# Kernel tuning notes

Hardware: AMD Instinct MI355X
Metric: run time of the kernel (lower is better)

The kernel has to match this reference:

```python
import jax, jax.numpy as jnp
import numpy as np

N_NODES = 50000
N_FEAT = 128
HIDDEN = 3
N_EDGES = 600000
N_POWERS = 3


def setup_inputs() -> dict:
    key = jax.random.key(0)
    ks = jax.random.split(key, 6)
    x = jax.random.normal(ks[0], (N_NODES, N_FEAT), dtype=jnp.float32)
    edge_index = jax.random.randint(ks[1], (N_POWERS, 2, N_EDGES), 0, N_NODES, dtype=jnp.int64)
    # MLP params for the 3 adjacency powers, stacked on the leading axis.
    # torch Linear(in,out) stored transposed here: y = x @ W + b.
    Wa = jax.random.normal(ks[2], (N_POWERS, N_FEAT, HIDDEN), dtype=jnp.float32) * (1.0 / np.sqrt(N_FEAT))
    ba = jax.random.normal(ks[3], (N_POWERS, HIDDEN), dtype=jnp.float32) * 0.01
    Wb = jax.random.normal(ks[4], (N_POWERS, HIDDEN, 1), dtype=jnp.float32) * (1.0 / np.sqrt(HIDDEN))
    bb = jax.random.normal(ks[5], (N_POWERS, 1), dtype=jnp.float32) * 0.01
    return {"x": x, "edge_index": edge_index, "Wa": Wa, "ba": ba, "Wb": Wb, "bb": bb}


def reference(x, edge_index, Wa, ba, Wb, bb):
    # Gather source/target node features per edge, per adjacency power.
    x_j = x[edge_index[:, 0]]          # [P, E, F]
    x_i = x[edge_index[:, 1]]          # [P, E, F]
    abs_dif = jnp.abs(x_j - x_i)       # [P, E, F]
    # Tiny per-edge MLP: Linear -> ReLU -> Linear -> Sigmoid (separate params per power).
    h = jax.nn.relu(jnp.einsum('pef,pfh->peh', abs_dif, Wa) + ba[:, None, :])  # [P, E, H]
    w = jax.nn.sigmoid(jnp.einsum('peh,pho->peo', h, Wb) + bb[:, None, :])     # [P, E, 1]
    return w[..., 0]                   # [P, E] edge weights for each power
```

## Files before the change

### kernel.cpp

```cpp
#include <hip/hip_runtime.h>
#include <math.h>

#define N_NODES 50000
#define N_FEAT  128
#define N_EDGES 600000
#define N_POWERS 3

#define ITERS 25
#define EDGES_PER_BLK (32 * ITERS)

typedef _Float16 half2v __attribute__((ext_vector_type(2)));
union HU { unsigned u; half2v h; };

__global__ __launch_bounds__(256) void conv_x(const float* __restrict__ x,
                                              unsigned* __restrict__ xh) {
    const int t = blockIdx.x * 256 + threadIdx.x;
    const float4* x4 = (const float4*)x;
    float4 a = x4[(size_t)t * 2];
    float4 b = x4[(size_t)t * 2 + 1];
    HU p0, p1, p2, p3;
    p0.h = half2v{(_Float16)a.x, (_Float16)a.y};
    p1.h = half2v{(_Float16)a.z, (_Float16)a.w};
    p2.h = half2v{(_Float16)b.x, (_Float16)b.y};
    p3.h = half2v{(_Float16)b.z, (_Float16)b.w};
    ((uint4*)xh)[t] = uint4{p0.u, p1.u, p2.u, p3.u};
}

__global__ __launch_bounds__(192) void conv_wa(const float* __restrict__ Wa,
                                               unsigned* __restrict__ wah) {
    const int t = blockIdx.x * 192 + threadIdx.x;
    const int c  = t % 3;
    const int pk = t / 3;
    const int k  = pk % 64;
    const int p  = pk / 64;
    float w0 = Wa[p * 384 + (2 * k) * 3 + c];
    float w1 = Wa[p * 384 + (2 * k + 1) * 3 + c];
    HU u; u.h = half2v{(_Float16)w0, (_Float16)w1};
    wah[t] = u.u;
}

template<int PAT>
__device__ __forceinline__ float swz(float v) {
    return __int_as_float(__builtin_amdgcn_ds_swizzle(__float_as_int(v), PAT));
}

__global__ __launch_bounds__(256) void adj_kernel_f16(
    const unsigned* __restrict__ xh,
    const unsigned* __restrict__ wah,
    const int*   __restrict__ edge_index,
    const float* __restrict__ ba,
    const float* __restrict__ Wb,
    const float* __restrict__ bb,
    float* __restrict__ out)
{
    const int p    = blockIdx.y;
    const int tid  = threadIdx.x;
    const int lane = tid & 63;
    const int wave = tid >> 6;
    const int sub  = lane & 7;
    const int grp  = lane >> 3;

    HU wa[8][3];
    {
        const unsigned* wp = wah + ((size_t)p * 64 + sub * 8) * 3;
        #pragma unroll
        for (int k = 0; k < 8; ++k) {
            wa[k][0].u = wp[k * 3 + 0];
            wa[k][1].u = wp[k * 3 + 1];
            wa[k][2].u = wp[k * 3 + 2];
        }
    }

    const float ba0 = ba[p * 3 + 0], ba1 = ba[p * 3 + 1], ba2 = ba[p * 3 + 2];
    const float wb0 = Wb[p * 3 + 0], wb1 = Wb[p * 3 + 1], wb2 = Wb[p * 3 + 2];
    const float bbp = bb[p];

    const int* ej = edge_index + (size_t)p * 2 * N_EDGES;
    const int* ei = ej + N_EDGES;
    float* outp = out + (size_t)p * N_EDGES;

    const int e_blk = blockIdx.x * EDGES_PER_BLK;
    const int eoff  = wave * 8 + grp;
    const int roff  = sub * 8;

    for (int it = 0; it < ITERS; ++it) {
        const int e = e_blk + it * 32 + eoff;
        const int j = ej[e];
        const int i = ei[e];

        const unsigned* rj = xh + (size_t)j * 64 + roff;
        const unsigned* ri = xh + (size_t)i * 64 + roff;
        uint4 qa0 = *(const uint4*)(rj);
        uint4 qa1 = *(const uint4*)(rj + 4);
        uint4 qb0 = *(const uint4*)(ri);
        uint4 qb1 = *(const uint4*)(ri + 4);

        unsigned ua[8] = {qa0.x, qa0.y, qa0.z, qa0.w, qa1.x, qa1.y, qa1.z, qa1.w};
        unsigned ub[8] = {qb0.x, qb0.y, qb0.z, qb0.w, qb1.x, qb1.y, qb1.z, qb1.w};

        float h0 = 0.f, h1 = 0.f, h2 = 0.f;
        #pragma unroll
        for (int k = 0; k < 8; ++k) {
            HU a, b, d;
            a.u = ua[k]; b.u = ub[k];
            d.h = a.h - b.h;
            d.u &= 0x7fff7fffu;
            h0 = __builtin_amdgcn_fdot2(d.h, wa[k][0].h, h0, false);
            h1 = __builtin_amdgcn_fdot2(d.h, wa[k][1].h, h1, false);
            h2 = __builtin_amdgcn_fdot2(d.h, wa[k][2].h, h2, false);
        }

        h0 += swz<0x041F>(h0); h1 += swz<0x041F>(h1); h2 += swz<0x041F>(h2);
        h0 += swz<0x081F>(h0); h1 += swz<0x081F>(h1); h2 += swz<0x081F>(h2);
        h0 += swz<0x101F>(h0); h1 += swz<0x101F>(h1); h2 += swz<0x101F>(h2);

        if (sub == 0) {
            float r0 = fmaxf(h0 + ba0, 0.f);
            float r1 = fmaxf(h1 + ba1, 0.f);
            float r2 = fmaxf(h2 + ba2, 0.f);
            float s  = fmaf(r0, wb0, fmaf(r1, wb1, fmaf(r2, wb2, bbp)));
            outp[e] = 1.f / (1.f + expf(-s));
        }
    }
}

__global__ __launch_bounds__(256) void adj_kernel_f32(
    const float* __restrict__ x,
    const int*   __restrict__ edge_index,
    const float* __restrict__ Wa,
    const float* __restrict__ ba,
    const float* __restrict__ Wb,
    const float* __restrict__ bb,
    float* __restrict__ out)
{
    const int p    = blockIdx.y;
    const int tid  = threadIdx.x;
    const int lane = tid & 63;
    const int wave = tid >> 6;
    const int sub  = lane & 15;
    const int grp  = lane >> 4;
    const int f0 = sub * 8;

    const float* Wap = Wa + (size_t)p * N_FEAT * 3;
    float wa0[8], wa1[8], wa2[8];
    #pragma unroll
    for (int k = 0; k < 8; ++k) {
        wa0[k] = Wap[(f0 + k) * 3 + 0];
        wa1[k] = Wap[(f0 + k) * 3 + 1];
        wa2[k] = Wap[(f0 + k) * 3 + 2];
    }
    const float ba0 = ba[p * 3 + 0], ba1 = ba[p * 3 + 1], ba2 = ba[p * 3 + 2];
    const float wb0 = Wb[p * 3 + 0], wb1 = Wb[p * 3 + 1], wb2 = Wb[p * 3 + 2];
    const float bbp = bb[p];

    const int e = blockIdx.x * 16 + wave * 4 + grp;
    const int* ej = edge_index + (size_t)p * 2 * N_EDGES;
    const int* ei = ej + N_EDGES;
    const int j = ej[e];
    const int i = ei[e];

    const float4* xj = (const float4*)(x + (size_t)j * N_FEAT + f0);
    const float4* xi = (const float4*)(x + (size_t)i * N_FEAT + f0);
    float4 a0 = xj[0], a1 = xj[1];
    float4 b0 = xi[0], b1 = xi[1];

    float d[8];
    d[0] = fabsf(a0.x - b0.x); d[1] = fabsf(a0.y - b0.y);
    d[2] = fabsf(a0.z - b0.z); d[3] = fabsf(a0.w - b0.w);
    d[4] = fabsf(a1.x - b1.x); d[5] = fabsf(a1.y - b1.y);
    d[6] = fabsf(a1.z - b1.z); d[7] = fabsf(a1.w - b1.w);

    float h0 = 0.f, h1 = 0.f, h2 = 0.f;
    #pragma unroll
    for (int k = 0; k < 8; ++k) {
        h0 = fmaf(d[k], wa0[k], h0);
        h1 = fmaf(d[k], wa1[k], h1);
        h2 = fmaf(d[k], wa2[k], h2);
    }
    #pragma unroll
    for (int m = 1; m < 16; m <<= 1) {
        h0 += __shfl_xor(h0, m, 64);
        h1 += __shfl_xor(h1, m, 64);
        h2 += __shfl_xor(h2, m, 64);
    }
    if (sub == 0) {
        float r0 = fmaxf(h0 + ba0, 0.f);
        float r1 = fmaxf(h1 + ba1, 0.f);
        float r2 = fmaxf(h2 + ba2, 0.f);
        float s  = fmaf(r0, wb0, fmaf(r1, wb1, fmaf(r2, wb2, bbp)));
        float w  = 1.f / (1.f + expf(-s));
        out[(size_t)p * N_EDGES + e] = w;
    }
}

extern "C" void kernel_launch(void* const* d_in, const int* in_sizes, int n_in,
                              void* d_out, int out_size, void* d_ws, size_t ws_size,
                              hipStream_t stream) {
    const float* x          = (const float*)d_in[0];
    const int*   edge_index = (const int*)d_in[1];
    const float* Wa         = (const float*)d_in[2];
    const float* ba         = (const float*)d_in[3];
    const float* Wb         = (const float*)d_in[4];
    const float* bb         = (const float*)d_in[5];
    float* out = (float*)d_out;

    const size_t x_bytes  = (size_t)N_NODES * N_FEAT * 2;
    const size_t wa_bytes = (size_t)N_POWERS * 64 * 3 * 4;
    if (ws_size >= x_bytes + wa_bytes) {
        unsigned* xh  = (unsigned*)d_ws;
        unsigned* wah = (unsigned*)((char*)d_ws + x_bytes);
        conv_x<<<(N_NODES * N_FEAT / 8 + 255) / 256, 256, 0, stream>>>(x, xh);
        conv_wa<<<3, 192, 0, stream>>>(Wa, wah);
        dim3 grid(N_EDGES / EDGES_PER_BLK, N_POWERS);
        adj_kernel_f16<<<grid, 256, 0, stream>>>(xh, wah, edge_index, ba, Wb, bb, out);
    } else {
        dim3 grid((N_EDGES + 15) / 16, N_POWERS);
        adj_kernel_f32<<<grid, 256, 0, stream>>>(x, edge_index, Wa, ba, Wb, bb, out);
    }
}
```

Before: 185.8 us.

## Process two edges per iteration with full unroll and smaller blocks

Each loop iteration now handles two edges, issuing all eight row gathers before computing, so more loads are in flight per wave. Blocks shrink from 800 to 320 edges, giving more blocks across the GPU, and the loop is fully unrolled. Edge-index loads and output stores become nontemporal, expf is replaced by the fast __expf, and an empty asm pins the weights in registers. The cost is higher register pressure from two live edge pipelines and slightly lower precision in the sigmoid.

Measured after the change: 180.4 us. -2.9%, faster.

```diff
diff --git a/kernel.cpp b/kernel.cpp
--- a/kernel.cpp
+++ b/kernel.cpp
@@ -6,8 +6,8 @@
 #define N_EDGES 600000
 #define N_POWERS 3
 
-#define ITERS 25
-#define EDGES_PER_BLK (32 * ITERS)
+#define PAIRS 5
+#define EDGES_PER_BLK (64 * PAIRS)
 
 typedef _Float16 half2v __attribute__((ext_vector_type(2)));
 union HU { unsigned u; half2v h; };
@@ -42,6 +42,25 @@
 template<int PAT>
 __device__ __forceinline__ float swz(float v) {
     return __int_as_float(__builtin_amdgcn_ds_swizzle(__float_as_int(v), PAT));
+}
+
+__device__ __forceinline__ void dot3_8(const uint4& qa0, const uint4& qa1,
+                                       const uint4& qb0, const uint4& qb1,
+                                       const HU wa[8][3],
+                                       float& h0, float& h1, float& h2) {
+    unsigned ua[8] = {qa0.x, qa0.y, qa0.z, qa0.w, qa1.x, qa1.y, qa1.z, qa1.w};
+    unsigned ub[8] = {qb0.x, qb0.y, qb0.z, qb0.w, qb1.x, qb1.y, qb1.z, qb1.w};
+    h0 = 0.f; h1 = 0.f; h2 = 0.f;
+    #pragma unroll
+    for (int k = 0; k < 8; ++k) {
+        HU a, b, d;
+        a.u = ua[k]; b.u = ub[k];
+        d.h = a.h - b.h;
+        d.u &= 0x7fff7fffu;
+        h0 = __builtin_amdgcn_fdot2(d.h, wa[k][0].h, h0, false);
+        h1 = __builtin_amdgcn_fdot2(d.h, wa[k][1].h, h1, false);
+        h2 = __builtin_amdgcn_fdot2(d.h, wa[k][2].h, h2, false);
+    }
 }
 
 __global__ __launch_bounds__(256) void adj_kernel_f16(
@@ -69,6 +88,10 @@
             wa[k][1].u = wp[k * 3 + 1];
             wa[k][2].u = wp[k * 3 + 2];
         }
+        #pragma unroll
+        for (int k = 0; k < 8; ++k) {
+            asm volatile("" : "+v"(wa[k][0].u), "+v"(wa[k][1].u), "+v"(wa[k][2].u));
+        }
     }
 
     const float ba0 = ba[p * 3 + 0], ba1 = ba[p * 3 + 1], ba2 = ba[p * 3 + 2];
@@ -83,43 +106,48 @@
     const int eoff  = wave * 8 + grp;
     const int roff  = sub * 8;
 
-    for (int it = 0; it < ITERS; ++it) {
-        const int e = e_blk + it * 32 + eoff;
-        const int j = ej[e];
-        const int i = ei[e];
-
-        const unsigned* rj = xh + (size_t)j * 64 + roff;
-        const unsigned* ri = xh + (size_t)i * 64 + roff;
-        uint4 qa0 = *(const uint4*)(rj);
-        uint4 qa1 = *(const uint4*)(rj + 4);
-        uint4 qb0 = *(const uint4*)(ri);
-        uint4 qb1 = *(const uint4*)(ri + 4);
-
-        unsigned ua[8] = {qa0.x, qa0.y, qa0.z, qa0.w, qa1.x, qa1.y, qa1.z, qa1.w};
-        unsigned ub[8] = {qb0.x, qb0.y, qb0.z, qb0.w, qb1.x, qb1.y, qb1.z, qb1.w};
-
-        float h0 = 0.f, h1 = 0.f, h2 = 0.f;
-        #pragma unroll
-        for (int k = 0; k < 8; ++k) {
-            HU a, b, d;
-            a.u = ua[k]; b.u = ub[k];
-            d.h = a.h - b.h;
-            d.u &= 0x7fff7fffu;
-            h0 = __builtin_amdgcn_fdot2(d.h, wa[k][0].h, h0, false);
-            h1 = __builtin_amdgcn_fdot2(d.h, wa[k][1].h, h1, false);
-            h2 = __builtin_amdgcn_fdot2(d.h, wa[k][2].h, h2, false);
-        }
-
-        h0 += swz<0x041F>(h0); h1 += swz<0x041F>(h1); h2 += swz<0x041F>(h2);
-        h0 += swz<0x081F>(h0); h1 += swz<0x081F>(h1); h2 += swz<0x081F>(h2);
-        h0 += swz<0x101F>(h0); h1 += swz<0x101F>(h1); h2 += swz<0x101F>(h2);
+    #pragma unroll
+    for (int it = 0; it < PAIRS; ++it) {
+        const int e1 = e_blk + it * 64 + eoff;
+        const int e2 = e1 + 32;
+
+        const int j1 = __builtin_nontemporal_load(ej + e1);
+        const int i1 = __builtin_nontemporal_load(ei + e1);
+        const int j2 = __builtin_nontemporal_load(ej + e2);
+        const int i2 = __builtin_nontemporal_load(ei + e2);
+
+        const uint4* rj1 = (const uint4*)(xh + ((size_t)j1 << 6) + roff);
+        const uint4* ri1 = (const uint4*)(xh + ((size_t)i1 << 6) + roff);
+        const uint4* rj2 = (const uint4*)(xh + ((size_t)j2 << 6) + roff);
+        const uint4* ri2 = (const uint4*)(xh + ((size_t)i2 << 6) + roff);
+        uint4 a0 = rj1[0], a1 = rj1[1];
+        uint4 b0 = ri1[0], b1 = ri1[1];
+        uint4 c0 = rj2[0], c1 = rj2[1];
+        uint4 d0 = ri2[0], d1 = ri2[1];
+
+        float h0a, h1a, h2a, h0b, h1b, h2b;
+        dot3_8(a0, a1, b0, b1, wa, h0a, h1a, h2a);
+        dot3_8(c0, c1, d0, d1, wa, h0b, h1b, h2b);
+
+        h0a += swz<0x041F>(h0a); h1a += swz<0x041F>(h1a); h2a += swz<0x041F>(h2a);
+        h0b += swz<0x041F>(h0b); h1b += swz<0x041F>(h1b); h2b += swz<0x041F>(h2b);
+        h0a += swz<0x081F>(h0a); h1a += swz<0x081F>(h1a); h2a += swz<0x081F>(h2a);
+        h0b += swz<0x081F>(h0b); h1b += swz<0x081F>(h1b); h2b += swz<0x081F>(h2b);
+        h0a += swz<0x101F>(h0a); h1a += swz<0x101F>(h1a); h2a += swz<0x101F>(h2a);
+        h0b += swz<0x101F>(h0b); h1b += swz<0x101F>(h1b); h2b += swz<0x101F>(h2b);
 
         if (sub == 0) {
-            float r0 = fmaxf(h0 + ba0, 0.f);
-            float r1 = fmaxf(h1 + ba1, 0.f);
-            float r2 = fmaxf(h2 + ba2, 0.f);
+            float r0 = fmaxf(h0a + ba0, 0.f);
+            float r1 = fmaxf(h1a + ba1, 0.f);
+            float r2 = fmaxf(h2a + ba2, 0.f);
             float s  = fmaf(r0, wb0, fmaf(r1, wb1, fmaf(r2, wb2, bbp)));
-            outp[e] = 1.f / (1.f + expf(-s));
+            __builtin_nontemporal_store(1.f / (1.f + __expf(-s)), outp + e1);
+
+            r0 = fmaxf(h0b + ba0, 0.f);
+            r1 = fmaxf(h1b + ba1, 0.f);
+            r2 = fmaxf(h2b + ba2, 0.f);
+            s  = fmaf(r0, wb0, fmaf(r1, wb1, fmaf(r2, wb2, bbp)));
+            __builtin_nontemporal_store(1.f / (1.f + __expf(-s)), outp + e2);
         }
     }
 }
```
